# Performance work log

Measured on AMD Instinct MI355X. Metric: run time of the kernel, lower is better.

Reference implementation:

```python
import jax, jax.numpy as jnp
import numpy as np

EPS = 1e-5

def _bn(x, g, b):
    # BatchNorm1d in training mode: biased batch variance, eps=1e-5
    mu = jnp.mean(x, axis=0)
    var = jnp.var(x, axis=0)
    return g * (x - mu) * jax.lax.rsqrt(var + EPS) + b

def _prelu(x, a):
    return jnp.where(x >= 0, x, a * x)

def setup_inputs() -> dict:
    key = jax.random.key(0)
    ks = jax.random.split(key, 32)
    B, MF, E = 4096, 128, 64
    f32 = jnp.float32

    def lin_w(k, o, i):
        bound = 1.0 / np.sqrt(i)
        return jax.random.uniform(k, (o, i), f32, -bound, bound)

    def lin_b(k, o, i):
        bound = 1.0 / np.sqrt(i)
        return jax.random.uniform(k, (o,), f32, -bound, bound)

    def exp_w(k, e, o, i):
        bound = 1.0 / np.sqrt(i)
        return jax.random.uniform(k, (e, o, i), f32, -bound, bound)

    def exp_b(k, e, o, i):
        bound = 1.0 / np.sqrt(i)
        return jax.random.uniform(k, (e, o), f32, -bound, bound)

    quarter = jnp.full((1,), 0.25, f32)  # PReLU default init
    return {
        'm0': jax.random.normal(ks[0], (B, MF), f32),
        'x0': jax.random.normal(ks[1], (B, 64), f32),
        'mW1': lin_w(ks[2], 256, 128), 'mb1': lin_b(ks[3], 256, 128),
        'mg1': jnp.ones((256,), f32), 'mbe1': jnp.zeros((256,), f32), 'ma1': quarter,
        'mW2': lin_w(ks[4], 128, 256), 'mb2': lin_b(ks[5], 128, 256),
        'mg2': jnp.ones((128,), f32), 'mbe2': jnp.zeros((128,), f32), 'ma2': quarter,
        'mW3': lin_w(ks[6], 64, 128), 'mb3': lin_b(ks[7], 64, 128),
        'mg3': jnp.ones((64,), f32), 'mbe3': jnp.zeros((64,), f32), 'ma3': quarter,
        'Wenc0': exp_w(ks[8], E, 256, 64), 'benc0': exp_b(ks[9], E, 256, 64),
        'Wenc1': exp_w(ks[10], E, 256, 256), 'benc1': exp_b(ks[11], E, 256, 256),
        'Wdec0': exp_w(ks[12], E, 256, 256), 'bdec0': exp_b(ks[13], E, 256, 256),
        'Wdec1': exp_w(ks[14], E, 64, 256), 'bdec1': exp_b(ks[15], E, 64, 256),
        'bng': jnp.ones((256,), f32), 'bnb': jnp.zeros((256,), f32), 'a': quarter,
    }

def reference(m0, x0, mW1, mb1, mg1, mbe1, ma1, mW2, mb2, mg2, mbe2, ma2,
              mW3, mb3, mg3, mbe3, ma3, Wenc0, benc0, Wenc1, benc1,
              Wdec0, bdec0, Wdec1, bdec1, bng, bnb, a):
    # m_encoder (MNet): Linear+BN+PReLU x3 -> per-sample expert weights [B, 64]
    h = _prelu(_bn(m0 @ mW1.T + mb1, mg1, mbe1), ma1)
    h = _prelu(_bn(h @ mW2.T + mb2, mg2, mbe2), ma2)
    w = _prelu(_bn(h @ mW3.T + mb3, mg3, mbe3), ma3)  # [B, E]

    w_sum = jnp.sum(w)           # scalar sum over all B*E, as in torch code
    wn = w / w_sum               # [B, E]

    def experts(z, W, b):
        # all-experts dense combine: sum_e wn[b,e] * (z @ W_e^T + b_e)
        h = jnp.einsum('bi,eoi->beo', z, W) + b  # [B, E, O]
        return jnp.einsum('beo,be->bo', h, wn)

    # encoder: depth=2, BN+PReLU after each layer (shared bn(256) and PReLU)
    z = _prelu(_bn(experts(x0, Wenc0, benc0), bng, bnb), a)
    z = _prelu(_bn(experts(z, Wenc1, benc1), bng, bnb), a)
    # decoder: BN+PReLU on all but last layer
    y = _prelu(_bn(experts(z, Wdec0, bdec0), bng, bnb), a)
    y = experts(y, Wdec1, bdec1)  # [B, 64]
    return y
```

## Files before the change

kernel.cpp:

```cpp
#include <hip/hip_runtime.h>
#include <stdint.h>

#define BATCH 4096
#define NEXP 64

typedef __bf16 bf16x8 __attribute__((ext_vector_type(8)));
typedef float f32x4 __attribute__((ext_vector_type(4)));
typedef float f32x8 __attribute__((ext_vector_type(8)));
typedef unsigned int u32x4 __attribute__((ext_vector_type(4)));
typedef unsigned short u16x4 __attribute__((ext_vector_type(4)));
typedef unsigned short u16x8 __attribute__((ext_vector_type(8)));

__device__ __forceinline__ unsigned short f2bf(float f) {
  unsigned u = __builtin_bit_cast(unsigned, f);
  u += 0x7fffu + ((u >> 16) & 1u);
  return (unsigned short)(u >> 16);
}
__device__ __forceinline__ float bf2f(unsigned short h) {
  unsigned u = ((unsigned)h) << 16;
  return __builtin_bit_cast(float, u);
}

__device__ __forceinline__ void async_copy16(const void* g, void* l) {
  __builtin_amdgcn_global_load_lds(
      (const __attribute__((address_space(1))) void*)(uintptr_t)g,
      (__attribute__((address_space(3))) void*)(uintptr_t)l, 16, 0, 0);
}

enum { AM_PLAIN = 0, AM_BN = 1, AM_EXPERT = 2 };

template <int BM_, int BN_, int WR, int WC, int AMODE>
__global__ __launch_bounds__(256, 4) void gemm_k(
    const float* __restrict__ Af32, const float* __restrict__ scv,
    const float* __restrict__ shv, const float* __restrict__ alphaPtr,
    const unsigned short* __restrict__ zbf, const unsigned short* __restrict__ wnb,
    int shI, int EI,
    const unsigned short* __restrict__ PB, int K, int nsubsTot,
    float* __restrict__ Cbase, long partStride,
    const float* __restrict__ biasv, int N, int ktilesTot, int splits) {
  constexpr int BK = 64;
  constexpr int MS = BM_ / 16;
  constexpr int NS = BN_ / 16;
  constexpr int WTM = BM_ / WR, WTN = BN_ / WC;
  constexpr int TM = WTM / 16, TN = WTN / 16;
  constexpr int PCH = MS / 2;

  __shared__ __align__(16) unsigned short As[2 * MS * 512];
  __shared__ __align__(16) unsigned short Bs[2 * NS * 512];

  const int tid = threadIdx.x;
  const int lane = tid & 63;
  const int wid = tid >> 6;
  const int wrow = wid / WC, wcol = wid % WC;

  const int m0 = blockIdx.x * BM_;
  const int ntile = blockIdx.y;
  const int n0 = ntile * BN_;
  const int slice = blockIdx.z;
  const int kt0 = (int)((long)slice * ktilesTot / splits);
  const int kt1 = (int)((long)(slice + 1) * ktilesTot / splits);

  float* __restrict__ Cp = Cbase + (long)slice * partStride;

  float alpha = 0.f;
  if constexpr (AMODE == AM_BN) alpha = alphaPtr[0];

  f32x4 acc[TM][TN] = {};

  for (int kt = kt0; kt < kt1; ++kt) {
    const int k0 = kt * BK;

    for (int f = wid; f < 2 * NS; f += 4) {
      const int fkt = f / NS, fns = f % NS;
      const long fragIdx = (long)(k0 / 32 + fkt) * nsubsTot + (ntile * NS + fns);
      async_copy16(PB + fragIdx * 512 + lane * 8, &Bs[f * 512 + lane * 8]);
    }

#pragma unroll
    for (int p = 0; p < PCH; ++p) {
      const int id = p * 256 + tid;
      const int fA = id >> 6;
      const int q = id & 63;
      const int ksh = fA / MS, msub = fA % MS;
      const int kq = q >> 4, mrow = q & 15;
      const int m = msub * 16 + mrow;
      const int kg = k0 + ksh * 32 + kq * 8;
      const long mg = m0 + m;
      f32x8 vf;
      if constexpr (AMODE == AM_PLAIN) {
        const f32x4* src = (const f32x4*)(Af32 + mg * K + kg);
        f32x4 a0 = src[0], a1 = src[1];
#pragma unroll
        for (int j = 0; j < 4; ++j) { vf[j] = a0[j]; vf[4 + j] = a1[j]; }
      } else {
        const f32x4* src = (const f32x4*)(Af32 + mg * K + kg);
        f32x4 a0 = src[0], a1 = src[1];
        f32x4 s0 = *(const f32x4*)(scv + kg), s1 = *(const f32x4*)(scv + kg + 4);
        f32x4 h0 = *(const f32x4*)(shv + kg), h1 = *(const f32x4*)(shv + kg + 4);
#pragma unroll
        for (int j = 0; j < 4; ++j) {
          float v = fmaf(a0[j], s0[j], h0[j]);
          vf[j] = v >= 0.f ? v : alpha * v;
          float v2 = fmaf(a1[j], s1[j], h1[j]);
          vf[4 + j] = v2 >= 0.f ? v2 : alpha * v2;
        }
      }
      bf16x8 ob = __builtin_convertvector(vf, bf16x8);
      *(u16x8*)&As[id * 8] = __builtin_bit_cast(u16x8, ob);
    }
    __syncthreads();

#pragma unroll
    for (int ks = 0; ks < 2; ++ks) {
      bf16x8 af[TM], bfr[TN];
#pragma unroll
      for (int i = 0; i < TM; ++i) {
        const int msub = wrow * TM + i;
        af[i] = __builtin_bit_cast(
            bf16x8, *(const u32x4*)&As[(ks * MS + msub) * 512 + lane * 8]);
      }
#pragma unroll
      for (int j = 0; j < TN; ++j) {
        const int nsub = wcol * TN + j;
        bfr[j] = __builtin_bit_cast(
            bf16x8, *(const u32x4*)&Bs[(ks * NS + nsub) * 512 + lane * 8]);
      }
#pragma unroll
      for (int i = 0; i < TM; ++i)
#pragma unroll
        for (int j = 0; j < TN; ++j)
          acc[i][j] = __builtin_amdgcn_mfma_f32_16x16x32_bf16(af[i], bfr[j],
                                                              acc[i][j], 0, 0, 0);
    }
    __syncthreads();
  }

  const int q = lane >> 4, nn = lane & 15;
#pragma unroll
  for (int i = 0; i < TM; ++i) {
    const int rowb = m0 + wrow * WTM + i * 16 + q * 4;
#pragma unroll
    for (int j = 0; j < TN; ++j) {
      const int col = n0 + wcol * WTN + j * 16 + nn;
      const float bv = biasv ? biasv[col] : 0.f;
#pragma unroll
      for (int r = 0; r < 4; ++r)
        Cp[(long)(rowb + r) * N + col] = acc[i][j][r] + bv;
    }
  }
  (void)zbf; (void)wnb; (void)shI; (void)EI;
}

template <int BN_, int KE_, int KSTG_>
__global__ __launch_bounds__(256, 3) void egemm_k(
    const unsigned short* __restrict__ zpk, const float* __restrict__ wnT,
    const float* __restrict__ bias, const unsigned short* __restrict__ PB,
    float* __restrict__ Cbase, long partStride, int N, int nsubsTot,
    int splits) {
  constexpr int KT2 = KE_ / 32;
  constexpr int NS = BN_ / 16;
  constexpr int NSTG = KT2 / KSTG_;
  constexpr int TM = 2, TN = NS / 2;
  constexpr int MS = 4;
  constexpr int WTN = BN_ / 2;

  __shared__ __align__(16) unsigned short Bs[KSTG_ * NS * 512];

  const int tid = threadIdx.x, lane = tid & 63, wid = tid >> 6;
  const int wrow = wid >> 1, wcol = wid & 1;
  const int mb = blockIdx.x, ntile = blockIdx.y, slice = blockIdx.z;
  const int epb = NEXP / splits, e0 = slice * epb;
  const int n0 = ntile * BN_;
  float* __restrict__ Cp = Cbase + (long)slice * partStride;
  const int nn = lane & 15, q = lane >> 4;

  u32x4 areg[TM][KT2];
  {
    const unsigned short* zb = zpk + (long)mb * (KT2 * MS * 512);
#pragma unroll
    for (int i = 0; i < TM; ++i) {
      const int msub = wrow * TM + i;
#pragma unroll
      for (int kt = 0; kt < KT2; ++kt)
        areg[i][kt] = *(const u32x4*)(zb + (kt * MS + msub) * 512 + lane * 8);
    }
  }

  f32x4 mainAcc[TM][TN] = {};

  for (int ei = 0; ei < epb; ++ei) {
    const int e = e0 + ei;

    float bv[TN];
#pragma unroll
    for (int j = 0; j < TN; ++j)
      bv[j] = bias[(long)e * N + n0 + wcol * WTN + j * 16 + nn];
    f32x4 tmp[TM][TN];
#pragma unroll
    for (int i = 0; i < TM; ++i)
#pragma unroll
      for (int j = 0; j < TN; ++j) {
        f32x4 t = {bv[j], bv[j], bv[j], bv[j]};
        tmp[i][j] = t;
      }

#pragma unroll
    for (int st = 0; st < NSTG; ++st) {
      for (int f = wid; f < KSTG_ * NS; f += 4) {
        const int kloc = f / NS, ns = f % NS;
        const long fragIdx =
            ((long)e * KT2 + st * KSTG_ + kloc) * nsubsTot + (ntile * NS + ns);
        async_copy16(PB + fragIdx * 512 + lane * 8, &Bs[f * 512 + lane * 8]);
      }
      __syncthreads();
#pragma unroll
      for (int kk = 0; kk < KSTG_; ++kk) {
        bf16x8 bfr[TN];
#pragma unroll
        for (int j = 0; j < TN; ++j)
          bfr[j] = __builtin_bit_cast(
              bf16x8,
              *(const u32x4*)&Bs[(kk * NS + wcol * TN + j) * 512 + lane * 8]);
        const int ktloc = st * KSTG_ + kk;
#pragma unroll
        for (int i = 0; i < TM; ++i) {
          bf16x8 af = __builtin_bit_cast(bf16x8, areg[i][ktloc]);
#pragma unroll
          for (int j = 0; j < TN; ++j)
            tmp[i][j] = __builtin_amdgcn_mfma_f32_16x16x32_bf16(
                af, bfr[j], tmp[i][j], 0, 0, 0);
        }
      }
      __syncthreads();
    }

#pragma unroll
    for (int i = 0; i < TM; ++i) {
      const int rowb = mb * 64 + wrow * 32 + i * 16 + q * 4;
      f32x4 wn4 = *(const f32x4*)(wnT + (long)e * BATCH + rowb);
#pragma unroll
      for (int j = 0; j < TN; ++j) mainAcc[i][j] += wn4 * tmp[i][j];
    }
  }

#pragma unroll
  for (int i = 0; i < TM; ++i) {
    const int rowb = mb * 64 + wrow * 32 + i * 16 + q * 4;
#pragma unroll
    for (int j = 0; j < TN; ++j) {
      const int col = n0 + wcol * WTN + j * 16 + nn;
#pragma unroll
      for (int r = 0; r < 4; ++r)
        Cp[(long)(rowb + r) * N + col] = mainAcc[i][j][r];
    }
  }
}

__global__ void hbuild_k(float* __restrict__ P, long partStride, int nparts,
                         int total4) {
  const int idx = blockIdx.x * 256 + threadIdx.x;
  if (idx >= total4) return;
  f32x4 s = *(const f32x4*)(P + (long)idx * 4);
  for (int p = 1; p < nparts; ++p)
    s += *(const f32x4*)(P + p * partStride + (long)idx * 4);
  *(f32x4*)(P + (long)idx * 4) = s;
}

__global__ void stats_k(const float* __restrict__ H, int C,
                        const float* __restrict__ g, const float* __restrict__ b,
                        float* __restrict__ scv, float* __restrict__ shv) {
  const int c0 = blockIdx.x * 4;
  f32x4 s = {0.f, 0.f, 0.f, 0.f}, s2 = {0.f, 0.f, 0.f, 0.f};
  for (int r = threadIdx.x; r < BATCH; r += 256) {
    f32x4 x = *(const f32x4*)(H + (long)r * C + c0);
    s += x;
    s2 += x * x;
  }
  __shared__ f32x4 sb[256], qb[256];
  sb[threadIdx.x] = s;
  qb[threadIdx.x] = s2;
  __syncthreads();
  for (int st = 128; st > 0; st >>= 1) {
    if (threadIdx.x < st) {
      sb[threadIdx.x] += sb[threadIdx.x + st];
      qb[threadIdx.x] += qb[threadIdx.x + st];
    }
    __syncthreads();
  }
  if (threadIdx.x < 4) {
    const int c = c0 + threadIdx.x;
    float mu = sb[0][threadIdx.x] * (1.f / BATCH);
    float var = qb[0][threadIdx.x] * (1.f / BATCH) - mu * mu;
    float isig = 1.f / sqrtf(var + 1e-5f);
    float sc_ = g[c] * isig;
    scv[c] = sc_;
    shv[c] = b[c] - mu * sc_;
  }
}

__global__ void zbuild_pk(const float* __restrict__ H,
                          const float* __restrict__ scv,
                          const float* __restrict__ shv,
                          const float* __restrict__ alphaPtr,
                          unsigned short* __restrict__ zpk) {
  const int c = blockIdx.x * 256 + threadIdx.x;
  const float alpha = alphaPtr[0];
  const int mb = c >> 11, r = c & 2047;
  const int kt = r >> 8, q2 = r & 255;
  const int msub = q2 >> 6, ln = q2 & 63;
  const int row = mb * 64 + msub * 16 + (ln & 15);
  const int col = kt * 32 + (ln >> 4) * 8;
  const float* src = H + (long)row * 256 + col;
  f32x4 a0 = *(const f32x4*)src, a1 = *(const f32x4*)(src + 4);
  f32x4 s0 = *(const f32x4*)(scv + col), s1 = *(const f32x4*)(scv + col + 4);
  f32x4 h0 = *(const f32x4*)(shv + col), h1 = *(const f32x4*)(shv + col + 4);
  u16x8 o;
#pragma unroll
  for (int j = 0; j < 4; ++j) {
    float v = fmaf(a0[j], s0[j], h0[j]);
    v = v >= 0.f ? v : alpha * v;
    o[j] = f2bf(v);
    float v2 = fmaf(a1[j], s1[j], h1[j]);
    v2 = v2 >= 0.f ? v2 : alpha * v2;
    o[4 + j] = f2bf(v2);
  }
  *(u16x8*)(zpk + (long)c * 8) = o;
}

__global__ void cast_pk(const float* __restrict__ x,
                        unsigned short* __restrict__ zpk) {
  const int c = blockIdx.x * 256 + threadIdx.x;
  const int mb = c >> 9, r = c & 511;
  const int kt = r >> 8, q2 = r & 255;
  const int msub = q2 >> 6, ln = q2 & 63;
  const int row = mb * 64 + msub * 16 + (ln & 15);
  const int col = kt * 32 + (ln >> 4) * 8;
  const float* src = x + (long)row * 64 + col;
  f32x4 a0 = *(const f32x4*)src, a1 = *(const f32x4*)(src + 4);
  u16x8 o;
#pragma unroll
  for (int j = 0; j < 4; ++j) {
    o[j] = f2bf(a0[j]);
    o[4 + j] = f2bf(a1[j]);
  }
  *(u16x8*)(zpk + (long)c * 8) = o;
}

__global__ void wbuild_k(const float* __restrict__ G, const float* __restrict__ scv,
                         const float* __restrict__ shv,
                         const float* __restrict__ alphaPtr,
                         float* __restrict__ w, float* __restrict__ wsum) {
  const int idx = blockIdx.x * 256 + threadIdx.x;
  const float alpha = alphaPtr[0];
  const int c0 = (idx * 4) & 63;
  f32x4 x = *(const f32x4*)(G + (long)idx * 4);
  f32x4 sv = *(const f32x4*)(scv + c0);
  f32x4 hv = *(const f32x4*)(shv + c0);
  f32x4 o;
  float part = 0.f;
#pragma unroll
  for (int j = 0; j < 4; ++j) {
    float v = fmaf(x[j], sv[j], hv[j]);
    v = v >= 0.f ? v : alpha * v;
    o[j] = v;
    part += v;
  }
  *(f32x4*)(w + (long)idx * 4) = o;
  __shared__ float sb[256];
  sb[threadIdx.x] = part;
  __syncthreads();
  for (int st = 128; st > 0; st >>= 1) {
    if (threadIdx.x < st) sb[threadIdx.x] += sb[threadIdx.x + st];
    __syncthreads();
  }
  if (threadIdx.x == 0) atomicAdd(wsum, sb[0]);
}

__global__ void inv_k(const float* __restrict__ wsum, float* __restrict__ invp) {
  if (threadIdx.x == 0 && blockIdx.x == 0) invp[0] = 1.0f / wsum[0];
}

__global__ void wntbuild_k(const float* __restrict__ w,
                           const float* __restrict__ invp,
                           float* __restrict__ wnT) {
  const int idx = blockIdx.x * 256 + threadIdx.x;
  const int e = idx >> 12, b = idx & 4095;
  wnT[idx] = w[(long)b * NEXP + e] * invp[0];
}

__global__ void prepack_k(const float* __restrict__ W, const float* __restrict__ bias,
                          unsigned short* __restrict__ PB, int O, int shI, int EI,
                          long totalChunks) {
  const long t = (long)blockIdx.x * 256 + threadIdx.x;
  if (t >= totalChunks) return;
  const int lane = (int)(t & 63);
  const long frag = t >> 6;
  const int nsubs = O / 16;
  const int nsub = (int)(frag % nsubs);
  const long ktile = frag / nsubs;
  const int n = nsub * 16 + (lane & 15);
  const int k = (int)(ktile * 32 + (lane >> 4) * 8);
  u16x8 o;
  if (k < EI) {
    const int e = k >> shI;
    const int i0 = k & ((1 << shI) - 1);
    const float* src = W + ((long)e * O + n) * (1 << shI) + i0;
    f32x4 a0 = *(const f32x4*)src;
    f32x4 a1 = *(const f32x4*)(src + 4);
#pragma unroll
    for (int j = 0; j < 4; ++j) {
      o[j] = f2bf(a0[j]);
      o[4 + j] = f2bf(a1[j]);
    }
  } else {
#pragma unroll
    for (int j = 0; j < 8; ++j) {
      const int ee = k + j - EI;
      o[j] = f2bf(bias[(long)ee * O + n]);
    }
  }
  *(u16x8*)(PB + t * 8) = o;
}

__global__ void reduceN_k(const float* __restrict__ P, long partStride, int nparts,
                          float* __restrict__ out, int total4) {
  const int idx = blockIdx.x * 256 + threadIdx.x;
  if (idx >= total4) return;
  f32x4 s = {0.f, 0.f, 0.f, 0.f};
  for (int p = 0; p < nparts; ++p) s += *(const f32x4*)(P + p * partStride + (long)idx * 4);
  *(f32x4*)(out + (long)idx * 4) = s;
}

extern "C" void kernel_launch(void* const* d_in, const int* in_sizes, int n_in,
                              void* d_out, int out_size, void* d_ws, size_t ws_size,
                              hipStream_t stream) {
  const float* m0 = (const float*)d_in[0];
  const float* x0 = (const float*)d_in[1];
  const float* mW1 = (const float*)d_in[2];
  const float* mb1 = (const float*)d_in[3];
  const float* mg1 = (const float*)d_in[4];
  const float* mbe1 = (const float*)d_in[5];
  const float* ma1 = (const float*)d_in[6];
  const float* mW2 = (const float*)d_in[7];
  const float* mb2 = (const float*)d_in[8];
  const float* mg2 = (const float*)d_in[9];
  const float* mbe2 = (const float*)d_in[10];
  const float* ma2 = (const float*)d_in[11];
  const float* mW3 = (const float*)d_in[12];
  const float* mb3 = (const float*)d_in[13];
  const float* mg3 = (const float*)d_in[14];
  const float* mbe3 = (const float*)d_in[15];
  const float* ma3 = (const float*)d_in[16];
  const float* Wenc0 = (const float*)d_in[17];
  const float* benc0 = (const float*)d_in[18];
  const float* Wenc1 = (const float*)d_in[19];
  const float* benc1 = (const float*)d_in[20];
  const float* Wdec0 = (const float*)d_in[21];
  const float* bdec0 = (const float*)d_in[22];
  const float* Wdec1 = (const float*)d_in[23];
  const float* bdec1 = (const float*)d_in[24];
  const float* bng = (const float*)d_in[25];
  const float* bnb = (const float*)d_in[26];
  const float* aexp = (const float*)d_in[27];

  const bool big = ws_size >= (size_t)52 * 1024 * 1024;
  const int SPL = big ? 8 : 4;
  const int SPLD = big ? 16 : 8;

  char* base = (char*)d_ws;
  size_t off = 0;
  auto alloc = [&](size_t bytes) {
    void* p = base + off;
    off = (off + bytes + 255) & ~(size_t)255;
    return p;
  };
  unsigned short* PB = (unsigned short*)alloc(16448L * 256 * 2);
  float* Pb = (float*)alloc((size_t)SPL * BATCH * 256 * 4);
  float* P0 = Pb;
  float* P1 = Pb + (long)BATCH * 256;
  unsigned short* zApk = (unsigned short*)alloc(BATCH * 256 * 2);
  unsigned short* zBpk = (unsigned short*)alloc(BATCH * 256 * 2);
  unsigned short* x0pk = (unsigned short*)alloc(BATCH * 64 * 2);
  float* wbuf = (float*)alloc(BATCH * 64 * 4);
  float* wnT = (float*)alloc((size_t)NEXP * BATCH * 4);
  float* scv = (float*)alloc(256 * 4);
  float* shv = (float*)alloc(256 * 4);
  float* wsum = (float*)alloc(256);
  float* invp = (float*)alloc(256);

  const dim3 blk(256);
  const long PS = BATCH * 256;

  prepack_k<<<16, blk, 0, stream>>>(mW1, nullptr, PB, 256, 7, 128, 4096);
  gemm_k<64, 128, 2, 2, AM_PLAIN><<<dim3(64, 2, 1), blk, 0, stream>>>(
      m0, nullptr, nullptr, nullptr, nullptr, nullptr, 0, 0, PB, 128, 16,
      P0, 0, mb1, 256, 2, 1);
  stats_k<<<64, blk, 0, stream>>>(P0, 256, mg1, mbe1, scv, shv);

  prepack_k<<<16, blk, 0, stream>>>(mW2, nullptr, PB, 128, 8, 256, 4096);
  gemm_k<64, 128, 2, 2, AM_BN><<<dim3(64, 1, 1), blk, 0, stream>>>(
      P0, scv, shv, ma1, nullptr, nullptr, 0, 0, PB, 256, 8, P1, 0, mb2,
      128, 4, 1);
  stats_k<<<32, blk, 0, stream>>>(P1, 128, mg2, mbe2, scv, shv);

  prepack_k<<<4, blk, 0, stream>>>(mW3, nullptr, PB, 64, 7, 128, 1024);
  gemm_k<64, 64, 2, 2, AM_BN><<<dim3(64, 1, 1), blk, 0, stream>>>(
      P1, scv, shv, ma2, nullptr, nullptr, 0, 0, PB, 128, 4, P0, 0, mb3,
      64, 2, 1);
  stats_k<<<16, blk, 0, stream>>>(P0, 64, mg3, mbe3, scv, shv);

  hipMemsetAsync(wsum, 0, 4, stream);
  wbuild_k<<<256, blk, 0, stream>>>(P0, scv, shv, ma3, wbuf, wsum);
  inv_k<<<1, 64, 0, stream>>>(wsum, invp);
  wntbuild_k<<<1024, blk, 0, stream>>>(wbuf, invp, wnT);
  cast_pk<<<128, blk, 0, stream>>>(x0, x0pk);

  prepack_k<<<512, blk, 0, stream>>>(Wenc0, nullptr, PB, 256, 6, 4096, 131072);
  egemm_k<128, 64, 2><<<dim3(64, 2, SPL), blk, 0, stream>>>(
      x0pk, wnT, benc0, PB, Pb, PS, 256, 16, SPL);
  hbuild_k<<<1024, blk, 0, stream>>>(Pb, PS, SPL, 262144);
  stats_k<<<64, blk, 0, stream>>>(Pb, 256, bng, bnb, scv, shv);
  zbuild_pk<<<512, blk, 0, stream>>>(Pb, scv, shv, aexp, zApk);

  prepack_k<<<2048, blk, 0, stream>>>(Wenc1, nullptr, PB, 256, 8, 16384, 524288);
  egemm_k<128, 256, 4><<<dim3(64, 2, SPL), blk, 0, stream>>>(
      zApk, wnT, benc1, PB, Pb, PS, 256, 16, SPL);
  hbuild_k<<<1024, blk, 0, stream>>>(Pb, PS, SPL, 262144);
  stats_k<<<64, blk, 0, stream>>>(Pb, 256, bng, bnb, scv, shv);
  zbuild_pk<<<512, blk, 0, stream>>>(Pb, scv, shv, aexp, zBpk);

  prepack_k<<<2048, blk, 0, stream>>>(Wdec0, nullptr, PB, 256, 8, 16384, 524288);
  egemm_k<128, 256, 4><<<dim3(64, 2, SPL), blk, 0, stream>>>(
      zBpk, wnT, bdec0, PB, Pb, PS, 256, 16, SPL);
  hbuild_k<<<1024, blk, 0, stream>>>(Pb, PS, SPL, 262144);
  stats_k<<<64, blk, 0, stream>>>(Pb, 256, bng, bnb, scv, shv);
  zbuild_pk<<<512, blk, 0, stream>>>(Pb, scv, shv, aexp, zApk);

  prepack_k<<<512, blk, 0, stream>>>(Wdec1, nullptr, PB, 64, 8, 16384, 131072);
  egemm_k<64, 256, 4><<<dim3(64, 1, SPLD), blk, 0, stream>>>(
      zApk, wnT, bdec1, PB, Pb, (long)BATCH * 64, 64, 4, SPLD);
  reduceN_k<<<256, blk, 0, stream>>>(Pb, (long)BATCH * 64, SPLD, (float*)d_out, 65536);

  (void)in_sizes; (void)n_in; (void)out_size;
}
```

Measured before the change: 418.4 us.

## Stream expert weights into registers directly, dropping LDS staging in egemm

Result: faster. 409.2 us (-2.2%).

```diff
diff --git a/kernel.cpp b/kernel.cpp
--- a/kernel.cpp
+++ b/kernel.cpp
@@ -27,18 +27,15 @@
       (__attribute__((address_space(3))) void*)(uintptr_t)l, 16, 0, 0);
 }
 
-enum { AM_PLAIN = 0, AM_BN = 1, AM_EXPERT = 2 };
+enum { AM_PLAIN = 0, AM_BN = 1 };
 
 template <int BM_, int BN_, int WR, int WC, int AMODE>
 __global__ __launch_bounds__(256, 4) void gemm_k(
     const float* __restrict__ Af32, const float* __restrict__ scv,
     const float* __restrict__ shv, const float* __restrict__ alphaPtr,
-    const unsigned short* __restrict__ zbf, const unsigned short* __restrict__ wnb,
-    int shI, int EI,
     const unsigned short* __restrict__ PB, int K, int nsubsTot,
-    float* __restrict__ Cbase, long partStride,
-    const float* __restrict__ biasv, int N, int ktilesTot, int splits) {
-  constexpr int BK = 64;
+    float* __restrict__ Cp, const float* __restrict__ biasv, int N,
+    int ktilesTot) {
   constexpr int MS = BM_ / 16;
   constexpr int NS = BN_ / 16;
   constexpr int WTM = BM_ / WR, WTN = BN_ / WC;
@@ -56,19 +53,14 @@
   const int m0 = blockIdx.x * BM_;
   const int ntile = blockIdx.y;
   const int n0 = ntile * BN_;
-  const int slice = blockIdx.z;
-  const int kt0 = (int)((long)slice * ktilesTot / splits);
-  const int kt1 = (int)((long)(slice + 1) * ktilesTot / splits);
-
-  float* __restrict__ Cp = Cbase + (long)slice * partStride;
 
   float alpha = 0.f;
   if constexpr (AMODE == AM_BN) alpha = alphaPtr[0];
 
   f32x4 acc[TM][TN] = {};
 
-  for (int kt = kt0; kt < kt1; ++kt) {
-    const int k0 = kt * BK;
+  for (int kt = 0; kt < ktilesTot; ++kt) {
+    const int k0 = kt * 64;
 
     for (int f = wid; f < 2 * NS; f += 4) {
       const int fkt = f / NS, fns = f % NS;
@@ -148,28 +140,22 @@
         Cp[(long)(rowb + r) * N + col] = acc[i][j][r] + bv;
     }
   }
-  (void)zbf; (void)wnb; (void)shI; (void)EI;
-}
-
-template <int BN_, int KE_, int KSTG_>
-__global__ __launch_bounds__(256, 3) void egemm_k(
+}
+
+template <int BN_, int KE_, int EPB>
+__global__ __launch_bounds__(256, 2) void egemm_k(
     const unsigned short* __restrict__ zpk, const float* __restrict__ wnT,
     const float* __restrict__ bias, const unsigned short* __restrict__ PB,
-    float* __restrict__ Cbase, long partStride, int N, int nsubsTot,
-    int splits) {
+    float* __restrict__ Cbase, long partStride, int N, int nsubsTot) {
   constexpr int KT2 = KE_ / 32;
   constexpr int NS = BN_ / 16;
-  constexpr int NSTG = KT2 / KSTG_;
-  constexpr int TM = 2, TN = NS / 2;
+  constexpr int TN = NS / 4;
+  constexpr int TM = 4;
   constexpr int MS = 4;
-  constexpr int WTN = BN_ / 2;
-
-  __shared__ __align__(16) unsigned short Bs[KSTG_ * NS * 512];
 
   const int tid = threadIdx.x, lane = tid & 63, wid = tid >> 6;
-  const int wrow = wid >> 1, wcol = wid & 1;
   const int mb = blockIdx.x, ntile = blockIdx.y, slice = blockIdx.z;
-  const int epb = NEXP / splits, e0 = slice * epb;
+  const int e0 = slice * EPB;
   const int n0 = ntile * BN_;
   float* __restrict__ Cp = Cbase + (long)slice * partStride;
   const int nn = lane & 15, q = lane >> 4;
@@ -178,23 +164,28 @@
   {
     const unsigned short* zb = zpk + (long)mb * (KT2 * MS * 512);
 #pragma unroll
-    for (int i = 0; i < TM; ++i) {
-      const int msub = wrow * TM + i;
+    for (int i = 0; i < TM; ++i)
 #pragma unroll
       for (int kt = 0; kt < KT2; ++kt)
-        areg[i][kt] = *(const u32x4*)(zb + (kt * MS + msub) * 512 + lane * 8);
-    }
-  }
+        areg[i][kt] = *(const u32x4*)(zb + (kt * MS + i) * 512 + lane * 8);
+  }
+
+  const unsigned short* Bw = PB + ((long)ntile * NS + wid * TN) * 512 + lane * 8;
+  const long kstride = (long)nsubsTot * 512;
 
   f32x4 mainAcc[TM][TN] = {};
-
-  for (int ei = 0; ei < epb; ++ei) {
+  u32x4 breg[2][TN];
+
+#pragma unroll
+  for (int j = 0; j < TN; ++j)
+    breg[0][j] = *(const u32x4*)(Bw + (long)e0 * KT2 * kstride + j * 512);
+
+  for (int ei = 0; ei < EPB; ++ei) {
     const int e = e0 + ei;
-
     float bv[TN];
 #pragma unroll
     for (int j = 0; j < TN; ++j)
-      bv[j] = bias[(long)e * N + n0 + wcol * WTN + j * 16 + nn];
+      bv[j] = bias[(long)e * N + n0 + wid * (TN * 16) + j * 16 + nn];
     f32x4 tmp[TM][TN];
 #pragma unroll
     for (int i = 0; i < TM; ++i)
@@ -203,40 +194,27 @@
         f32x4 t = {bv[j], bv[j], bv[j], bv[j]};
         tmp[i][j] = t;
       }
-
-#pragma unroll
-    for (int st = 0; st < NSTG; ++st) {
-      for (int f = wid; f < KSTG_ * NS; f += 4) {
-        const int kloc = f / NS, ns = f % NS;
-        const long fragIdx =
-            ((long)e * KT2 + st * KSTG_ + kloc) * nsubsTot + (ntile * NS + ns);
-        async_copy16(PB + fragIdx * 512 + lane * 8, &Bs[f * 512 + lane * 8]);
+#pragma unroll
+    for (int kt = 0; kt < KT2; ++kt) {
+      const int cur = kt & 1, nxt = cur ^ 1;
+      if (kt + 1 < KT2 || ei + 1 < EPB) {
+        const long tnext = (long)e * KT2 + kt + 1;
+#pragma unroll
+        for (int j = 0; j < TN; ++j)
+          breg[nxt][j] = *(const u32x4*)(Bw + tnext * kstride + j * 512);
       }
-      __syncthreads();
-#pragma unroll
-      for (int kk = 0; kk < KSTG_; ++kk) {
-        bf16x8 bfr[TN];
+#pragma unroll
+      for (int i = 0; i < TM; ++i) {
+        bf16x8 af = __builtin_bit_cast(bf16x8, areg[i][kt]);
 #pragma unroll
         for (int j = 0; j < TN; ++j)
-          bfr[j] = __builtin_bit_cast(
-              bf16x8,
-              *(const u32x4*)&Bs[(kk * NS + wcol * TN + j) * 512 + lane * 8]);
-        const int ktloc = st * KSTG_ + kk;
-#pragma unroll
-        for (int i = 0; i < TM; ++i) {
-          bf16x8 af = __builtin_bit_cast(bf16x8, areg[i][ktloc]);
-#pragma unroll
-          for (int j = 0; j < TN; ++j)
-            tmp[i][j] = __builtin_amdgcn_mfma_f32_16x16x32_bf16(
-                af, bfr[j], tmp[i][j], 0, 0, 0);
-        }
+          tmp[i][j] = __builtin_amdgcn_mfma_f32_16x16x32_bf16(
+              af, __builtin_bit_cast(bf16x8, breg[cur][j]), tmp[i][j], 0, 0, 0);
       }
-      __syncthreads();
-    }
-
+    }
 #pragma unroll
     for (int i = 0; i < TM; ++i) {
-      const int rowb = mb * 64 + wrow * 32 + i * 16 + q * 4;
+      const int rowb = mb * 64 + i * 16 + q * 4;
       f32x4 wn4 = *(const f32x4*)(wnT + (long)e * BATCH + rowb);
 #pragma unroll
       for (int j = 0; j < TN; ++j) mainAcc[i][j] += wn4 * tmp[i][j];
@@ -245,10 +223,10 @@
 
 #pragma unroll
   for (int i = 0; i < TM; ++i) {
-    const int rowb = mb * 64 + wrow * 32 + i * 16 + q * 4;
+    const int rowb = mb * 64 + i * 16 + q * 4;
 #pragma unroll
     for (int j = 0; j < TN; ++j) {
-      const int col = n0 + wcol * WTN + j * 16 + nn;
+      const int col = n0 + wid * (TN * 16) + j * 16 + nn;
 #pragma unroll
       for (int r = 0; r < 4; ++r)
         Cp[(long)(rowb + r) * N + col] = mainAcc[i][j][r];
@@ -463,9 +441,7 @@
   const float* bnb = (const float*)d_in[26];
   const float* aexp = (const float*)d_in[27];
 
-  const bool big = ws_size >= (size_t)52 * 1024 * 1024;
-  const int SPL = big ? 8 : 4;
-  const int SPLD = big ? 16 : 8;
+  const int SPL = 4, SPLD = 8;
 
   char* base = (char*)d_ws;
   size_t off = 0;
@@ -493,20 +469,17 @@
 
   prepack_k<<<16, blk, 0, stream>>>(mW1, nullptr, PB, 256, 7, 128, 4096);
   gemm_k<64, 128, 2, 2, AM_PLAIN><<<dim3(64, 2, 1), blk, 0, stream>>>(
-      m0, nullptr, nullptr, nullptr, nullptr, nullptr, 0, 0, PB, 128, 16,
-      P0, 0, mb1, 256, 2, 1);
+      m0, nullptr, nullptr, nullptr, PB, 128, 16, P0, mb1, 256, 2);
   stats_k<<<64, blk, 0, stream>>>(P0, 256, mg1, mbe1, scv, shv);
 
   prepack_k<<<16, blk, 0, stream>>>(mW2, nullptr, PB, 128, 8, 256, 4096);
   gemm_k<64, 128, 2, 2, AM_BN><<<dim3(64, 1, 1), blk, 0, stream>>>(
-      P0, scv, shv, ma1, nullptr, nullptr, 0, 0, PB, 256, 8, P1, 0, mb2,
-      128, 4, 1);
+      P0, scv, shv, ma1, PB, 256, 8, P1, mb2, 128, 4);
   stats_k<<<32, blk, 0, stream>>>(P1, 128, mg2, mbe2, scv, shv);
 
   prepack_k<<<4, blk, 0, stream>>>(mW3, nullptr, PB, 64, 7, 128, 1024);
   gemm_k<64, 64, 2, 2, AM_BN><<<dim3(64, 1, 1), blk, 0, stream>>>(
-      P1, scv, shv, ma2, nullptr, nullptr, 0, 0, PB, 128, 4, P0, 0, mb3,
-      64, 2, 1);
+      P1, scv, shv, ma2, PB, 128, 4, P0, mb3, 64, 2);
   stats_k<<<16, blk, 0, stream>>>(P0, 64, mg3, mbe3, scv, shv);
 
   hipMemsetAsync(wsum, 0, 4, stream);
@@ -516,30 +489,30 @@
   cast_pk<<<128, blk, 0, stream>>>(x0, x0pk);
 
   prepack_k<<<512, blk, 0, stream>>>(Wenc0, nullptr, PB, 256, 6, 4096, 131072);
-  egemm_k<128, 64, 2><<<dim3(64, 2, SPL), blk, 0, stream>>>(
-      x0pk, wnT, benc0, PB, Pb, PS, 256, 16, SPL);
+  egemm_k<128, 64, 16><<<dim3(64, 2, SPL), blk, 0, stream>>>(
+      x0pk, wnT, benc0, PB, Pb, PS, 256, 16);
   hbuild_k<<<1024, blk, 0, stream>>>(Pb, PS, SPL, 262144);
   stats_k<<<64, blk, 0, stream>>>(Pb, 256, bng, bnb, scv, shv);
   zbuild_pk<<<512, blk, 0, stream>>>(Pb, scv, shv, aexp, zApk);
 
   prepack_k<<<2048, blk, 0, stream>>>(Wenc1, nullptr, PB, 256, 8, 16384, 524288);
-  egemm_k<128, 256, 4><<<dim3(64, 2, SPL), blk, 0, stream>>>(
-      zApk, wnT, benc1, PB, Pb, PS, 256, 16, SPL);
+  egemm_k<128, 256, 16><<<dim3(64, 2, SPL), blk, 0, stream>>>(
+      zApk, wnT, benc1, PB, Pb, PS, 256, 16);
   hbuild_k<<<1024, blk, 0, stream>>>(Pb, PS, SPL, 262144);
   stats_k<<<64, blk, 0, stream>>>(Pb, 256, bng, bnb, scv, shv);
   zbuild_pk<<<512, blk, 0, stream>>>(Pb, scv, shv, aexp, zBpk);
 
   prepack_k<<<2048, blk, 0, stream>>>(Wdec0, nullptr, PB, 256, 8, 16384, 524288);
-  egemm_k<128, 256, 4><<<dim3(64, 2, SPL), blk, 0, stream>>>(
-      zBpk, wnT, bdec0, PB, Pb, PS, 256, 16, SPL);
+  egemm_k<128, 256, 16><<<dim3(64, 2, SPL), blk, 0, stream>>>(
+      zBpk, wnT, bdec0, PB, Pb, PS, 256, 16);
   hbuild_k<<<1024, blk, 0, stream>>>(Pb, PS, SPL, 262144);
   stats_k<<<64, blk, 0, stream>>>(Pb, 256, bng, bnb, scv, shv);
   zbuild_pk<<<512, blk, 0, stream>>>(Pb, scv, shv, aexp, zApk);
 
   prepack_k<<<512, blk, 0, stream>>>(Wdec1, nullptr, PB, 64, 8, 16384, 131072);
-  egemm_k<64, 256, 4><<<dim3(64, 1, SPLD), blk, 0, stream>>>(
-      zApk, wnT, bdec1, PB, Pb, (long)BATCH * 64, 64, 4, SPLD);
+  egemm_k<64, 256, 8><<<dim3(64, 1, SPLD), blk, 0, stream>>>(
+      zApk, wnT, bdec1, PB, Pb, (long)BATCH * 64, 64, 4);
   reduceN_k<<<256, blk, 0, stream>>>(Pb, (long)BATCH * 64, SPLD, (float*)d_out, 65536);
 
-  (void)in_sizes; (void)n_in; (void)out_size;
-}
+  (void)in_sizes; (void)n_in; (void)out_size; (void)ws_size;
+}
```
